# Optimization experiments

Measured on AMD Instinct MI355X. Metric: run time of the kernel, lower is better.

The kernel has to match this reference:

```python
import jax, jax.numpy as jnp
from jax import lax
import numpy as np

EPS = 1e-5

def _bn(x, g, b):
    # training-mode BatchNorm2d: batch stats over (N,H,W), biased variance
    m = jnp.mean(x, axis=(0, 2, 3), keepdims=True)
    v = jnp.var(x, axis=(0, 2, 3), keepdims=True)
    return g[None, :, None, None] * (x - m) * lax.rsqrt(v + EPS) + b[None, :, None, None]

def _conv(x, w, b, stride=1, pad=0):
    y = lax.conv_general_dilated(x, w, (stride, stride), [(pad, pad), (pad, pad)],
                                 dimension_numbers=('NCHW', 'OIHW', 'NCHW'))
    return y + b[None, :, None, None]

def _convT(x, w, b):
    # torch ConvTranspose2d(k=4, s=2, p=1); w: [in, out, 4, 4]
    wf = jnp.flip(w, (2, 3)).transpose(1, 0, 2, 3)  # -> [out, in, 4, 4]
    y = lax.conv_general_dilated(x, wf, (1, 1), [(2, 2), (2, 2)], lhs_dilation=(2, 2),
                                 dimension_numbers=('NCHW', 'OIHW', 'NCHW'))
    return y + b[None, :, None, None]

def setup_inputs() -> dict:
    key = jax.random.key(0)
    ks = jax.random.split(key, 16)
    B, C_IN, HW = 32, 3, 512
    H_ENC, H_LAT, HID, N_EMB = 16, 2, 64, 3  # Encoder/Decoder hidden, VQ hidden/embed_dim, vqvae hidden, codebook size
    r = lambda k, s: jax.random.normal(k, s, jnp.float32) * 0.05
    return {
        'x': jax.random.normal(ks[0], (B, C_IN, HW, HW), jnp.float32),
        'enc_w1': r(ks[1], (H_ENC, C_IN, 4, 4)), 'enc_b1': r(ks[2], (H_ENC,)),
        'enc_g1': jnp.ones((H_ENC,), jnp.float32), 'enc_be1': jnp.zeros((H_ENC,), jnp.float32),
        'enc_w2': r(ks[3], (HID, H_ENC, 4, 4)), 'enc_b2': r(ks[4], (HID,)),
        'enc_g2': jnp.ones((HID,), jnp.float32), 'enc_be2': jnp.zeros((HID,), jnp.float32),
        'preq_w': r(ks[5], (H_LAT, HID, 1, 1)), 'preq_b': r(ks[6], (H_LAT,)),
        'emb': r(ks[7], (N_EMB, H_LAT)),
        'postq_w': r(ks[8], (HID, H_LAT, 1, 1)), 'postq_b': r(ks[9], (HID,)),
        'dec_w1': r(ks[10], (HID, H_ENC, 4, 4)), 'dec_b1': r(ks[11], (H_ENC,)),
        'dec_g1': jnp.ones((H_ENC,), jnp.float32), 'dec_be1': jnp.zeros((H_ENC,), jnp.float32),
        'dec_w2': r(ks[12], (H_ENC, C_IN, 4, 4)), 'dec_b2': r(ks[13], (C_IN,)),
    }

def reference(x, enc_w1, enc_b1, enc_g1, enc_be1, enc_w2, enc_b2, enc_g2, enc_be2,
              preq_w, preq_b, emb, postq_w, postq_b,
              dec_w1, dec_b1, dec_g1, dec_be1, dec_w2, dec_b2):
    # Encoder
    h = jax.nn.relu(_bn(_conv(x, enc_w1, enc_b1, 2, 1), enc_g1, enc_be1))
    h = jax.nn.relu(_bn(_conv(h, enc_w2, enc_b2, 2, 1), enc_g2, enc_be2))
    # VQ latent space
    q = _conv(h, preq_w, preq_b)                       # [B, 2, H/4, W/4]
    Bq, Cq, Hq, Wq = q.shape
    qf = q.transpose(0, 2, 3, 1).reshape(Bq * Hq * Wq, Cq)
    # squared distances (argmin-equivalent to torch.cdist p=2)
    d2 = jnp.sum(qf**2, -1, keepdims=True) + jnp.sum(emb**2, -1)[None, :] - 2.0 * (qf @ emb.T)
    idx = jnp.argmin(d2, axis=-1)
    e = emb[idx]                                       # gather [N, 2]
    commit = jnp.mean((lax.stop_gradient(e) - qf) ** 2)
    codebook = jnp.mean((e - lax.stop_gradient(qf)) ** 2)
    qloss = codebook + 0.2 * commit
    qout = qf + lax.stop_gradient(e - qf)              # straight-through estimator
    qout = qout.reshape(Bq, Hq, Wq, Cq).transpose(0, 3, 1, 2)
    d = _conv(qout, postq_w, postq_b)
    # Decoder
    d = jax.nn.relu(_bn(_convT(d, dec_w1, dec_b1), dec_g1, dec_be1))
    recon = jnp.tanh(_convT(d, dec_w2, dec_b2))
    return recon, qloss
```

## Files before the change

kernel.cpp:

```cpp
#include <hip/hip_runtime.h>
#include <hip/hip_bf16.h>


#define EPSB 1e-5f

__device__ __forceinline__ float wredf(float v){
#pragma unroll
  for (int m = 32; m >= 1; m >>= 1) v += __shfl_xor(v, m, 64);
  return v;
}

__device__ __forceinline__ float fast_tanh(float x){
  float e = __expf(2.f * x);
  return fmaf(-2.f, __builtin_amdgcn_rcpf(e + 1.f), 1.f);
}

__global__ __launch_bounds__(256) void kP(
    const float* __restrict__ w1, const float* __restrict__ w2,
    const float* __restrict__ dw2,
    const float* __restrict__ pqw, const float* __restrict__ pqb,
    const float* __restrict__ emb,
    float* __restrict__ wt1, float* __restrict__ wt2,
    float* __restrict__ wt9, float* __restrict__ misc)
{
  const int b = blockIdx.x, t = threadIdx.x;
  const int s = b*256 + t;
  { int tap = s >> 6, co = s & 63;
    int ci = tap >> 4, ky = (tap >> 2) & 3, kx = tap & 3;
    wt2[s] = w2[((co*16 + ci)*4 + ky)*4 + kx]; }
  if (b == 0){
    for (int s2 = t; s2 < 768; s2 += 256){
      int tap = s2 >> 4, co = s2 & 15;
      int ci = tap >> 4, ky = (tap >> 2) & 3, kx = tap & 3;
      wt1[s2] = w1[((co*3 + ci)*4 + ky)*4 + kx];
      int ky9 = s2 / 192, rem = s2 - ky9*192;
      int ci9 = rem / 12, r12 = rem - ci9*12;
      int kx9 = r12 / 3, co9 = r12 - kx9*3;
      wt9[s2] = dw2[((ci9*3 + co9)*4 + ky9)*4 + kx9];
    }
    if (t < 192){
      int i = t >> 6, ci = t & 63;
      misc[200 + t] = fmaf(pqw[ci*2], emb[i*2],
                      fmaf(pqw[ci*2 + 1], emb[i*2 + 1], pqb[ci]));
    }
    if (t == 255) misc[192] = 0.f;
  }
}

__global__ __launch_bounds__(64) void k6b_tt(
    const float* __restrict__ dw1, float* __restrict__ misc)
{
  const int e = blockIdx.x;
  const int i = e >> 8, rem = e & 255;
  const int kykx = rem >> 4, oc = rem & 15;
  const int ky = kykx >> 2, kx = kykx & 3;
  const int l = threadIdx.x;
  float v = dw1[((l*16 + oc)*4 + ky)*4 + kx] * misc[200 + i*64 + l];
  v = wredf(v);
  if (l == 0) misc[400 + i*260 + rem] = v;
}

__global__ __launch_bounds__(256) void k1_conv1(
    const float* __restrict__ x, const float* __restrict__ wt1,
    float* __restrict__ h1p, float* __restrict__ part1)
{
  __shared__ __align__(16) float xt[3*6*516];
  __shared__ float red[128];
  const int b = blockIdx.x, t = threadIdx.x;
  const int n = b >> 7, yt = b & 127;
  const int oy0 = yt << 1, iy0 = (oy0 << 1) - 1;
  const int rh = t >> 7, l128 = t & 127, c4 = l128 << 2;
#pragma unroll
  for (int rp = 0; rp < 9; rp++){
    int rIdx = (rp << 1) + rh;
    int ci = rIdx / 6, rr = rIdx - ci*6;
    int iy = iy0 + rr;
    bool yok = (unsigned)iy < 512u;
    const float* xr = x + (((size_t)(n*3 + ci)) << 18) + ((size_t)(iy & 511) << 9);
    float* dst = &xt[rIdx*516];
    float4 v = make_float4(0.f, 0.f, 0.f, 0.f);
    if (yok) v = *(const float4*)&xr[c4];
    dst[c4 + 1] = v.x; dst[c4 + 2] = v.y; dst[c4 + 3] = v.z; dst[c4 + 4] = v.w;
    if (l128 == 0){ dst[0] = 0.f; dst[513] = 0.f; }
  }
  __syncthreads();
  const int w = t >> 6, l = t & 63;
  const int oyr = w & 1, xh = w >> 1;
  float acc[2][16];
#pragma unroll
  for (int j = 0; j < 2; j++)
#pragma unroll
    for (int q = 0; q < 16; q++) acc[j][q] = 0.f;

  for (int ci = 0; ci < 3; ci++){
    for (int ky = 0; ky < 4; ky++){
      const float* xrow = &xt[(ci*6 + (oyr << 1) + ky)*516];
      float v[2][4];
#pragma unroll
      for (int j = 0; j < 2; j++){
        int ox = (xh << 7) + (j << 6) + l;
        float2 p0 = *(const float2*)&xrow[2*ox];
        float2 p1 = *(const float2*)&xrow[2*ox + 2];
        v[j][0] = p0.x; v[j][1] = p0.y; v[j][2] = p1.x; v[j][3] = p1.y;
      }
      const float* wb = &wt1[((ci*4 + ky) << 6)];
#pragma unroll
      for (int kx = 0; kx < 4; kx++){
        const float* wp = wb + (kx << 4);
        float wv[16];
#pragma unroll
        for (int q = 0; q < 16; q++) wv[q] = wp[q];
#pragma unroll
        for (int j = 0; j < 2; j++)
#pragma unroll
          for (int q = 0; q < 16; q++) acc[j][q] = fmaf(v[j][kx], wv[q], acc[j][q]);
      }
    }
  }
  float s[16], ss[16];
#pragma unroll
  for (int q = 0; q < 16; q++){ s[q] = 0.f; ss[q] = 0.f; }
  const int xp = l & 1;
#pragma unroll
  for (int j = 0; j < 2; j++){
    int m = (xh << 6) + (j << 5) + (l >> 1);
#pragma unroll
    for (int q = 0; q < 16; q++){
      float vv = acc[j][q];
      h1p[((((size_t)(n*16 + q) << 1) + oyr) << 15) + ((size_t)xp << 14) + (yt << 7) + m] = vv;
      s[q] += vv; ss[q] += vv*vv;
    }
  }
#pragma unroll
  for (int q = 0; q < 16; q++){ s[q] = wredf(s[q]); ss[q] = wredf(ss[q]); }
  if (l == 0){
#pragma unroll
    for (int q = 0; q < 16; q++){ red[w*32 + q] = s[q]; red[w*32 + 16 + q] = ss[q]; }
  }
  __syncthreads();
  if (t < 32) part1[b*32 + t] = red[t] + red[32+t] + red[64+t] + red[96+t];
}

__global__ __launch_bounds__(256) void k_stats(
    const float* __restrict__ part, int nslots, int slotstride, int grouped,
    const float* __restrict__ g, const float* __restrict__ be,
    float* __restrict__ scale, float* __restrict__ shift, float Ninv)
{
  const int c = blockIdx.x, t = threadIdx.x;
  const int off = grouped ? ((c >> 4) << 5) : 0;
  const int ci = grouped ? (c & 15) : c;
  float S = 0.f, SS = 0.f;
  for (int q = t; q < nslots; q += 256){
    const float* pp = &part[(size_t)q * slotstride + off];
    S += pp[ci]; SS += pp[16 + ci];
  }
  S = wredf(S); SS = wredf(SS);
  __shared__ float sb[8];
  if ((t & 63) == 0){ sb[t >> 6] = S; sb[4 + (t >> 6)] = SS; }
  __syncthreads();
  if (t == 0){
    float Sv = sb[0]+sb[1]+sb[2]+sb[3], SSv = sb[4]+sb[5]+sb[6]+sb[7];
    float m = Sv * Ninv;
    float var = SSv * Ninv - m*m;
    float sc = g[c] * rsqrtf(var + EPSB);
    scale[c] = sc;
    shift[c] = be[c] - m * sc;
  }
}

__global__ __launch_bounds__(256) void k3_conv2(
    const float* __restrict__ h1p, const float* __restrict__ wt2,
    const float* __restrict__ misc, float* __restrict__ h2,
    float* __restrict__ part2)
{
  __shared__ __align__(16) float a1[6144];
  __shared__ float red[128];
  const int b = blockIdx.x, t = threadIdx.x;
  const int n = b >> 6, yt = b & 63;
  const int oy0 = yt << 1;
  const int w = __builtin_amdgcn_readfirstlane(t >> 6);
  const int l = t & 63, oyr = l >> 5, lx = l & 31;
  const int sxp = t >> 7, sm = t & 127;
  float acc[4][16];
#pragma unroll
  for (int e = 0; e < 4; e++)
#pragma unroll
    for (int q = 0; q < 16; q++) acc[e][q] = 0.f;

  float pf[24];
#define K3_PF(CC) { \
    const int cc_ = (CC); \
    _Pragma("unroll") \
    for (int r = 0; r < 24; r++){ \
      const int ys = r >> 2, ci = r & 3; \
      const int yp = (ys >= 3) ? 1 : 0; \
      const int dy = (ys >= 3) ? (ys - 4) : ys; \
      const int m_yc = (oy0 + dy) & 127; \
      pf[r] = h1p[((((size_t)(n*16 + (cc_ << 2) + ci)) << 1) + yp << 15) \
                  + ((size_t)sxp << 14) + (m_yc << 7) + sm]; \
    } }

  K3_PF(0);
  __builtin_amdgcn_sched_barrier(0);
  for (int cc = 0; cc < 4; cc++){
    __syncthreads();
#pragma unroll
    for (int r = 0; r < 24; r++){
      const int ys = r >> 2;
      const int dy = (ys >= 3) ? (ys - 4) : ys;
      const int m_y = oy0 + dy;
      const bool yok = (unsigned)m_y < 128u;
      const int gci = (cc << 2) + (r & 3);
      const float bnv = fmaxf(fmaf(pf[r], misc[gci], misc[16 + gci]), 0.f);
      a1[(r << 8) + t] = yok ? bnv : 0.f;
    }
    __syncthreads();
    if (cc < 3){
      K3_PF(cc + 1);
      __builtin_amdgcn_sched_barrier(0);
    }
    for (int cl = 0; cl < 4; cl++){
#pragma unroll
      for (int ky = 0; ky < 4; ky++){
        const int ys = (ky & 1) ? (oyr + (ky >> 1)) : (3 + oyr + (ky >> 1));
        const float* base = &a1[(((ys << 2) + cl)) << 8];
        float4 A0 = *(const float4*)(base + (lx << 2));
        float4 A1 = *(const float4*)(base + 128 + (lx << 2));
        float nx0 = __shfl_down(A0.x, 1, 64);  if (lx == 31) nx0 = 0.f;
        float pv1 = __shfl_up(A1.w, 1, 64);    if (lx == 0)  pv1 = 0.f;
        float act0[4] = {pv1,  A1.x, A1.y, A1.z};
        float act1[4] = {A0.x, A0.y, A0.z, A0.w};
        float act2[4] = {A1.x, A1.y, A1.z, A1.w};
        float act3[4] = {A0.y, A0.z, A0.w, nx0};
        const float* wb = &wt2[(((((cc << 2) + cl) << 4) + (ky << 2)) << 6) + (w << 4)];
#pragma unroll
        for (int kx = 0; kx < 4; kx++){
          const float* wp = wb + (kx << 6);
          float wv[16];
#pragma unroll
          for (int q = 0; q < 16; q++) wv[q] = wp[q];
          const float* av = (kx == 0) ? act0 : (kx == 1) ? act1 : (kx == 2) ? act2 : act3;
#pragma unroll
          for (int e = 0; e < 4; e++)
#pragma unroll
            for (int q = 0; q < 16; q++)
              acc[e][q] = fmaf(av[e], wv[q], acc[e][q]);
        }
      }
    }
  }
  const int oy = oy0 + oyr;
  float s[16], ss[16];
#pragma unroll
  for (int q = 0; q < 16; q++){ s[q] = 0.f; ss[q] = 0.f; }
#pragma unroll
  for (int e = 0; e < 4; e++)
#pragma unroll
    for (int q = 0; q < 16; q++){ float v = acc[e][q]; s[q] += v; ss[q] += v*v; }
#pragma unroll
  for (int q = 0; q < 16; q++){
    float4 o = make_float4(acc[0][q], acc[1][q], acc[2][q], acc[3][q]);
    *(float4*)&h2[(((size_t)(n*64) + (w << 4) + q) << 14) + (oy << 7) + (lx << 2)] = o;
  }
#pragma unroll
  for (int q = 0; q < 16; q++){ s[q] = wredf(s[q]); ss[q] = wredf(ss[q]); }
  if (l == 0){
#pragma unroll
    for (int q = 0; q < 16; q++){ red[w*32 + q] = s[q]; red[w*32 + 16 + q] = ss[q]; }
  }
  __syncthreads();
  if (t < 128) part2[b*128 + t] = red[t];
}

__global__ __launch_bounds__(256) void k5_vq(
    const float* __restrict__ h2, const float* __restrict__ misc,
    const float* __restrict__ pw, const float* __restrict__ pb,
    const float* __restrict__ emb, unsigned char* __restrict__ idxb,
    float* __restrict__ qsum)
{
  __shared__ float eb[4];
  const int t = threadIdx.x;
  const int p0 = blockIdx.x*512 + (t << 1);
  const int n = p0 >> 14, pos = p0 & 16383;
  const float* hp = h2 + ((size_t)n << 20) + pos;
  float q0[2], q1[2];
  const float pb0 = pb[0], pb1 = pb[1];
#pragma unroll
  for (int j = 0; j < 2; j++){ q0[j] = pb0; q1[j] = pb1; }
  for (int c = 0; c < 64; c++){
    float2 v = *(const float2*)&hp[(size_t)c << 14];
    float sc = misc[32 + c], sh = misc[96 + c];
    float w0 = pw[c], w1 = pw[64 + c];
    float a0 = fmaxf(fmaf(v.x, sc, sh), 0.f);
    float a1 = fmaxf(fmaf(v.y, sc, sh), 0.f);
    q0[0] = fmaf(a0, w0, q0[0]); q1[0] = fmaf(a0, w1, q1[0]);
    q0[1] = fmaf(a1, w0, q0[1]); q1[1] = fmaf(a1, w1, q1[1]);
  }
  const float e00 = emb[0], e01 = emb[1], e10 = emb[2], e11 = emb[3],
              e20 = emb[4], e21 = emb[5];
  float esum = 0.f;
  unsigned char bi[2];
#pragma unroll
  for (int j = 0; j < 2; j++){
    float dx0 = q0[j]-e00, dy0 = q1[j]-e01;
    float dx1 = q0[j]-e10, dy1 = q1[j]-e11;
    float dx2 = q0[j]-e20, dy2 = q1[j]-e21;
    float d0 = dx0*dx0+dy0*dy0, d1 = dx1*dx1+dy1*dy1, d2 = dx2*dx2+dy2*dy2;
    int bj = 0; float db = d0;
    if (d1 < db){ db = d1; bj = 1; }
    if (d2 < db){ db = d2; bj = 2; }
    bi[j] = (unsigned char)bj; esum += db;
  }
  *(uchar2*)&idxb[p0] = make_uchar2(bi[0], bi[1]);
  float e = wredf(esum);
  if ((t & 63) == 0) eb[t >> 6] = e;
  __syncthreads();
  if (t == 0) atomicAdd(qsum, eb[0]+eb[1]+eb[2]+eb[3]);
}

__device__ __forceinline__ void d1_accum(const unsigned char* __restrict__ ib,
    int iy, int ix, const float* __restrict__ tt, float* __restrict__ d)
{
  const int py = (iy + 1) & 1, px = (ix + 1) & 1;
#pragma unroll
  for (int kyi = 0; kyi < 2; kyi++){
    int ky = py + 2*kyi, jy = (iy + 1 - ky) >> 1;
    if ((unsigned)jy < 128u){
#pragma unroll
      for (int kxi = 0; kxi < 2; kxi++){
        int kx = px + 2*kxi, jx = (ix + 1 - kx) >> 1;
        if ((unsigned)jx < 128u){
          const float4* tb = (const float4*)&tt[(int)ib[(jy << 7) + jx]*260
                                                + (((ky << 2) + kx) << 4)];
          float4 t0 = tb[0], t1 = tb[1], t2 = tb[2], t3 = tb[3];
          d[0]  += t0.x; d[1]  += t0.y; d[2]  += t0.z; d[3]  += t0.w;
          d[4]  += t1.x; d[5]  += t1.y; d[6]  += t1.z; d[7]  += t1.w;
          d[8]  += t2.x; d[9]  += t2.y; d[10] += t2.z; d[11] += t2.w;
          d[12] += t3.x; d[13] += t3.y; d[14] += t3.z; d[15] += t3.w;
        }
      }
    }
  }
}

__global__ __launch_bounds__(256) void k7s(
    const unsigned char* __restrict__ idxb, const float* __restrict__ misc,
    float* __restrict__ partd, float* __restrict__ qout)
{
  __shared__ __align__(16) float tt[780];
  __shared__ float red[128];
  const int b = blockIdx.x, t = threadIdx.x;
  for (int s = t; s < 780; s += 256) tt[s] = misc[400 + s];
  __syncthreads();
  if (b == 0 && t == 0) qout[0] = 1.2f * misc[192] * (1.0f/1048576.0f);
  float s[16], ss[16];
#pragma unroll
  for (int q = 0; q < 16; q++){ s[q] = 0.f; ss[q] = 0.f; }
  for (int k = 0; k < 4; k++){
    int p = (b << 10) + (k << 8) + t;
    int n = p >> 16, rem = p & 65535, iy = rem >> 8, ix = rem & 255;
    const unsigned char* ib = idxb + ((size_t)n << 14);
    float d[16];
#pragma unroll
    for (int q = 0; q < 16; q++) d[q] = 0.f;
    d1_accum(ib, iy, ix, tt, d);
#pragma unroll
    for (int q = 0; q < 16; q++){ s[q] += d[q]; ss[q] += d[q]*d[q]; }
  }
#pragma unroll
  for (int q = 0; q < 16; q++){ s[q] = wredf(s[q]); ss[q] = wredf(ss[q]); }
  const int w = t >> 6, l = t & 63;
  if (l == 0){
#pragma unroll
    for (int q = 0; q < 16; q++){ red[w*32 + q] = s[q]; red[w*32 + 16 + q] = ss[q]; }
  }
  __syncthreads();
  if (t < 32) partd[b*32 + t] = red[t] + red[32+t] + red[64+t] + red[96+t];
}

__global__ __launch_bounds__(256) void k9_dec(
    const unsigned char* __restrict__ idxb, const float* __restrict__ misc,
    const float* __restrict__ wt9, const float* __restrict__ db2,
    float* __restrict__ out)
{
  __shared__ __align__(16) float a[4*16*132];
  __shared__ __align__(16) float tt[780];
  __shared__ float sd[16], shs[16];
  const int b = blockIdx.x, t = threadIdx.x;
  const int n = b >> 8, r8 = b & 255, G = r8 >> 1, xh = r8 & 1;
  const int M0 = xh << 7;
  for (int s = t; s < 780; s += 256) tt[s] = misc[400 + s];
  if (t < 16){ sd[t] = misc[160 + t]; shs[t] = misc[176 + t]; }
  __syncthreads();
  const unsigned char* ib = idxb + ((size_t)n << 14);
#pragma unroll
  for (int pass = 0; pass < 2; pass++){
    int s = t + (pass << 8);
    int iyr = s >> 7, col = s & 127;
    int iy = (G << 1) - 1 + iyr, ix = M0 + col - 1;
    bool inb = ((unsigned)iy < 256u) && ((unsigned)ix < 256u);
    float d[16];
#pragma unroll
    for (int q = 0; q < 16; q++) d[q] = 0.f;
    if (inb) d1_accum(ib, iy, ix, tt, d);
#pragma unroll
    for (int q = 0; q < 16; q++)
      a[(iyr*16 + q)*132 + col] = inb ? fmaxf(fmaf(d[q], sd[q], shs[q]), 0.f) : 0.f;
  }
  if (t < 8){
    int iyr = t >> 1, col = 128 + (t & 1);
    int iy = (G << 1) - 1 + iyr, ix = M0 + col - 1;
    bool inb = ((unsigned)iy < 256u) && ((unsigned)ix < 256u);
    float d[16];
#pragma unroll
    for (int q = 0; q < 16; q++) d[q] = 0.f;
    if (inb) d1_accum(ib, iy, ix, tt, d);
#pragma unroll
    for (int q = 0; q < 16; q++)
      a[(iyr*16 + q)*132 + col] = inb ? fmaxf(fmaf(d[q], sd[q], shs[q]), 0.f) : 0.f;
  }
  __syncthreads();
  const int rowq = t >> 6, u = t & 63;
  const int oy2 = (G << 2) + rowq;
  const int py = (oy2 + 1) & 1;
  float acc[2][2][3];
#pragma unroll
  for (int p2 = 0; p2 < 2; p2++)
#pragma unroll
    for (int e = 0; e < 2; e++)
#pragma unroll
      for (int c = 0; c < 3; c++) acc[p2][e][c] = 0.f;

#pragma unroll
  for (int kyi = 0; kyi < 2; kyi++){
    const int ky = py + (kyi << 1);
    const int iy = (oy2 + 1 - ky) >> 1;
    if ((unsigned)iy < 256u){
      const int iyr = iy - ((G << 1) - 1);
      for (int ci = 0; ci < 16; ci++){
        const float* wp = &wt9[(ky*16 + ci)*12];
        float w[12];
#pragma unroll
        for (int k = 0; k < 12; k++) w[k] = wp[k];
        const float* ar = &a[(iyr*16 + ci)*132];
        float2 c0 = *(const float2*)&ar[2*u];
        float2 c1 = *(const float2*)&ar[2*u + 2];
        float v[4] = {c0.x, c0.y, c1.x, c1.y};
#pragma unroll
        for (int e = 0; e < 2; e++){
          float vmm = v[e], v0m = v[e+1], vp1 = v[e+2];
          acc[1][e][0] = fmaf(vp1, w[0], acc[1][e][0]);
          acc[1][e][1] = fmaf(vp1, w[1], acc[1][e][1]);
          acc[1][e][2] = fmaf(vp1, w[2], acc[1][e][2]);
          acc[0][e][0] = fmaf(v0m, w[3], acc[0][e][0]);
          acc[0][e][1] = fmaf(v0m, w[4], acc[0][e][1]);
          acc[0][e][2] = fmaf(v0m, w[5], acc[0][e][2]);
          acc[1][e][0] = fmaf(v0m, w[6], acc[1][e][0]);
          acc[1][e][1] = fmaf(v0m, w[7], acc[1][e][1]);
          acc[1][e][2] = fmaf(v0m, w[8], acc[1][e][2]);
          acc[0][e][0] = fmaf(vmm, w[9], acc[0][e][0]);
          acc[0][e][1] = fmaf(vmm, w[10], acc[0][e][1]);
          acc[0][e][2] = fmaf(vmm, w[11], acc[0][e][2]);
        }
      }
    }
  }
  const float bb[3] = {db2[0], db2[1], db2[2]};
#pragma unroll
  for (int co = 0; co < 3; co++){
    float4 o = make_float4(fast_tanh(acc[0][0][co] + bb[co]), fast_tanh(acc[1][0][co] + bb[co]),
                           fast_tanh(acc[0][1][co] + bb[co]), fast_tanh(acc[1][1][co] + bb[co]));
    *(float4*)&out[((size_t)(n*3 + co) << 18) + ((size_t)oy2 << 9) + (M0 << 1) + (u << 2)] = o;
  }
}

extern "C" void kernel_launch(void* const* d_in, const int* in_sizes, int n_in,
                              void* d_out, int out_size, void* d_ws, size_t ws_size,
                              hipStream_t stream)
{
  (void)in_sizes; (void)n_in; (void)out_size;
  const float* x       = (const float*)d_in[0];
  const float* enc_w1  = (const float*)d_in[1];
  const float* enc_g1  = (const float*)d_in[3];
  const float* enc_be1 = (const float*)d_in[4];
  const float* enc_w2  = (const float*)d_in[5];
  const float* enc_g2  = (const float*)d_in[7];
  const float* enc_be2 = (const float*)d_in[8];
  const float* preq_w  = (const float*)d_in[9];
  const float* preq_b  = (const float*)d_in[10];
  const float* emb     = (const float*)d_in[11];
  const float* postq_w = (const float*)d_in[12];
  const float* postq_b = (const float*)d_in[13];
  const float* dec_w1  = (const float*)d_in[14];
  const float* dec_g1  = (const float*)d_in[16];
  const float* dec_be1 = (const float*)d_in[17];
  const float* dec_w2  = (const float*)d_in[18];
  const float* dec_b2  = (const float*)d_in[19];
  float* out = (float*)d_out;
  char*  ws  = (char*)d_ws;

  float* h1p = (float*)ws;
  float* h2  = (float*)(ws + 134217728);
  size_t ebase = (ws_size - 4194304) & ~(size_t)255;
  unsigned char* idxb = (unsigned char*)(ws + ebase);
  float* part1 = (float*)(ws + ebase + 524288);
  float* partd = (float*)(ws + ebase + 1048576);
  float* misc  = (float*)(ws + ebase + 1310720);
  float* wt1   = (float*)(ws + ebase + 1318912);
  float* wt2   = (float*)(ws + ebase + 1327104);
  float* wt9   = (float*)(ws + ebase + 1392640);
  float* part2 = out;

  kP<<<64, 256, 0, stream>>>(enc_w1, enc_w2, dec_w2,
                             postq_w, postq_b, emb, wt1, wt2, wt9, misc);
  k6b_tt<<<768, 64, 0, stream>>>(dec_w1, misc);
  k1_conv1<<<4096, 256, 0, stream>>>(x, wt1, h1p, part1);
  k_stats<<<16, 256, 0, stream>>>(part1, 4096, 32, 0, enc_g1, enc_be1,
                                  misc + 0, misc + 16, 1.f/2097152.f);
  k3_conv2<<<2048, 256, 0, stream>>>(h1p, wt2, misc, h2, part2);
  k_stats<<<64, 256, 0, stream>>>(part2, 2048, 128, 1, enc_g2, enc_be2,
                                  misc + 32, misc + 96, 1.f/524288.f);
  k5_vq<<<1024, 256, 0, stream>>>(h2, misc, preq_w, preq_b, emb, idxb, misc + 192);
  k7s<<<2048, 256, 0, stream>>>(idxb, misc, partd, out + 25165824);
  k_stats<<<16, 256, 0, stream>>>(partd, 2048, 32, 0, dec_g1, dec_be1,
                                  misc + 160, misc + 176, 1.f/2097152.f);
  k9_dec<<<8192, 256, 0, stream>>>(idxb, misc, wt9, dec_b2, out);
}
```

Baseline: 529.9 us.

## Stream conv2 input tiles to LDS via async DMA with double buffering

```diff
diff --git a/kernel.cpp b/kernel.cpp
--- a/kernel.cpp
+++ b/kernel.cpp
@@ -3,6 +3,9 @@
 
 
 #define EPSB 1e-5f
+
+typedef const __attribute__((address_space(1))) void GV;
+typedef __attribute__((address_space(3))) void LV;
 
 __device__ __forceinline__ float wredf(float v){
 #pragma unroll
@@ -173,65 +176,64 @@
     const float* __restrict__ misc, float* __restrict__ h2,
     float* __restrict__ part2)
 {
-  __shared__ __align__(16) float a1[6144];
+  __shared__ __align__(16) float a1[2][6144];
   __shared__ float red[128];
   const int b = blockIdx.x, t = threadIdx.x;
   const int n = b >> 6, yt = b & 63;
   const int oy0 = yt << 1;
   const int w = __builtin_amdgcn_readfirstlane(t >> 6);
   const int l = t & 63, oyr = l >> 5, lx = l & 31;
-  const int sxp = t >> 7, sm = t & 127;
+  const size_t lane_off = ((size_t)(l >> 5) << 14) + ((size_t)(l & 31) << 2);
   float acc[4][16];
 #pragma unroll
   for (int e = 0; e < 4; e++)
 #pragma unroll
     for (int q = 0; q < 16; q++) acc[e][q] = 0.f;
 
-  float pf[24];
-#define K3_PF(CC) { \
+#define K3_DMA(CC, BUFI) { \
     const int cc_ = (CC); \
     _Pragma("unroll") \
-    for (int r = 0; r < 24; r++){ \
-      const int ys = r >> 2, ci = r & 3; \
-      const int yp = (ys >= 3) ? 1 : 0; \
-      const int dy = (ys >= 3) ? (ys - 4) : ys; \
-      const int m_yc = (oy0 + dy) & 127; \
-      pf[r] = h1p[((((size_t)(n*16 + (cc_ << 2) + ci)) << 1) + yp << 15) \
-                  + ((size_t)sxp << 14) + (m_yc << 7) + sm]; \
+    for (int ys = 0; ys < 6; ys++){ \
+      const int yp_ = (ys >= 3) ? 1 : 0; \
+      const int dy_ = (ys >= 3) ? (ys - 4) : ys; \
+      const int myc_ = (oy0 + dy_) & 127; \
+      const float* g_ = h1p + (((((size_t)(n*16 + (cc_ << 2) + w)) << 1) + yp_) << 15) \
+                        + ((size_t)myc_ << 7) + lane_off; \
+      float* l_ = &a1[BUFI][(((ys << 2) + w) << 8)]; \
+      __builtin_amdgcn_global_load_lds((GV*)(const void*)g_, (LV*)(void*)l_, 16, 0, 0); \
     } }
 
-  K3_PF(0);
-  __builtin_amdgcn_sched_barrier(0);
+  K3_DMA(0, 0);
+  __syncthreads();
   for (int cc = 0; cc < 4; cc++){
-    __syncthreads();
-#pragma unroll
-    for (int r = 0; r < 24; r++){
-      const int ys = r >> 2;
-      const int dy = (ys >= 3) ? (ys - 4) : ys;
-      const int m_y = oy0 + dy;
-      const bool yok = (unsigned)m_y < 128u;
-      const int gci = (cc << 2) + (r & 3);
-      const float bnv = fmaxf(fmaf(pf[r], misc[gci], misc[16 + gci]), 0.f);
-      a1[(r << 8) + t] = yok ? bnv : 0.f;
-    }
-    __syncthreads();
-    if (cc < 3){
-      K3_PF(cc + 1);
-      __builtin_amdgcn_sched_barrier(0);
-    }
+    if (cc < 3) K3_DMA(cc + 1, (cc + 1) & 1);
+    const float* cur = a1[cc & 1];
     for (int cl = 0; cl < 4; cl++){
+      const int gci = (cc << 2) + cl;
+      const float sc = misc[gci], sh = misc[16 + gci];
 #pragma unroll
       for (int ky = 0; ky < 4; ky++){
         const int ys = (ky & 1) ? (oyr + (ky >> 1)) : (3 + oyr + (ky >> 1));
-        const float* base = &a1[(((ys << 2) + cl)) << 8];
-        float4 A0 = *(const float4*)(base + (lx << 2));
-        float4 A1 = *(const float4*)(base + 128 + (lx << 2));
-        float nx0 = __shfl_down(A0.x, 1, 64);  if (lx == 31) nx0 = 0.f;
-        float pv1 = __shfl_up(A1.w, 1, 64);    if (lx == 0)  pv1 = 0.f;
-        float act0[4] = {pv1,  A1.x, A1.y, A1.z};
-        float act1[4] = {A0.x, A0.y, A0.z, A0.w};
-        float act2[4] = {A1.x, A1.y, A1.z, A1.w};
-        float act3[4] = {A0.y, A0.z, A0.w, nx0};
+        const int dy = (ys >= 3) ? (ys - 4) : ys;
+        const bool rv = (unsigned)(oy0 + dy) < 128u;
+        const float scv = rv ? sc : 0.f, shv = rv ? sh : 0.f;
+        const float* base = &cur[(((ys << 2) + cl)) << 8];
+        float4 R0 = *(const float4*)(base + (lx << 2));
+        float4 R1 = *(const float4*)(base + 128 + (lx << 2));
+        float A0x = fmaxf(fmaf(R0.x, scv, shv), 0.f);
+        float A0y = fmaxf(fmaf(R0.y, scv, shv), 0.f);
+        float A0z = fmaxf(fmaf(R0.z, scv, shv), 0.f);
+        float A0w = fmaxf(fmaf(R0.w, scv, shv), 0.f);
+        float A1x = fmaxf(fmaf(R1.x, scv, shv), 0.f);
+        float A1y = fmaxf(fmaf(R1.y, scv, shv), 0.f);
+        float A1z = fmaxf(fmaf(R1.z, scv, shv), 0.f);
+        float A1w = fmaxf(fmaf(R1.w, scv, shv), 0.f);
+        float nx0 = __shfl_down(A0x, 1, 64);  if (lx == 31) nx0 = 0.f;
+        float pv1 = __shfl_up(A1w, 1, 64);    if (lx == 0)  pv1 = 0.f;
+        float act0[4] = {pv1, A1x, A1y, A1z};
+        float act1[4] = {A0x, A0y, A0z, A0w};
+        float act2[4] = {A1x, A1y, A1z, A1w};
+        float act3[4] = {A0y, A0z, A0w, nx0};
         const float* wb = &wt2[(((((cc << 2) + cl) << 4) + (ky << 2)) << 6) + (w << 4)];
 #pragma unroll
         for (int kx = 0; kx < 4; kx++){
@@ -248,6 +250,7 @@
         }
       }
     }
+    __syncthreads();
   }
   const int oy = oy0 + oyr;
   float s[16], ss[16];
```

Result: no change. 532.1 us (+0.4%).
